# Optimization experiments

Measured on AMD Instinct MI355X. Metric: run time of the kernel, lower is better.

The kernel has to match this reference:

```python
import jax, jax.numpy as jnp
import numpy as np

TEMPERATURE = 0.07
NEG_INF = -1e30


def setup_inputs() -> dict:
    key = jax.random.key(0)
    k_h, k_m, k_l, k_w = jax.random.split(key, 4)
    B, L, H, P = 32, 1024, 1280, 128
    hidden_states = jax.random.normal(k_h, (B, L, H), dtype=jnp.float32)
    attention_mask = jax.random.randint(k_m, (B, L), 0, 2).astype(jnp.int32)
    labels = jax.random.randint(k_l, (B, L), 0, 4).astype(jnp.int32)
    proj_w = jax.random.normal(k_w, (H, P), dtype=jnp.float32) * 0.02
    proj_b = jnp.zeros((P,), dtype=jnp.float32)
    return {
        "hidden_states": hidden_states,
        "proj_w": proj_w,
        "proj_b": proj_b,
        "attention_mask": attention_mask,
        "labels": labels,
    }


def reference(hidden_states, proj_w, proj_b, attention_mask, labels):
    # Projection head (dropout is inactive at eval) + L2 normalize
    emb = hidden_states @ proj_w + proj_b                     # [B, L, P]
    emb = emb / jnp.linalg.norm(emb, axis=-1, keepdims=True)

    B, L, _ = emb.shape
    attn_valid = attention_mask.astype(bool)                  # [B, L]
    valid = attn_valid & (labels != -100)                     # anchor/candidate validity

    # Per-sequence token-token similarity, temperature-scaled
    sim = jnp.einsum("bip,bjp->bij", emb, emb) / TEMPERATURE  # [B, L, L]

    eye = jnp.eye(L, dtype=bool)                              # [L, L]
    col_valid = valid[:, None, :]                             # valid candidate j
    # Row max over valid columns (includes self, as in original filtered emb)
    m = jax.lax.stop_gradient(
        jnp.max(jnp.where(col_valid, sim, NEG_INF), axis=2, keepdims=True)
    )
    logits = sim - m
    logits_mask = col_valid & ~eye[None]                      # exclude self, invalid cols
    exp_logits = jnp.where(logits_mask, jnp.exp(logits), 0.0)
    log_prob = logits - jnp.log(exp_logits.sum(axis=2, keepdims=True) + 1e-12)

    # Positives: same label, same sequence, not self, both valid
    same_label = labels[:, :, None] == labels[:, None, :]
    pos_mask = (same_label & logits_mask & valid[:, :, None]).astype(sim.dtype)

    sum_pos_log_prob = (pos_mask * log_prob).sum(axis=2)      # [B, L]
    anchor_loss = sum_pos_log_prob / (pos_mask.sum(axis=2) + 1e-12)

    valid_f = valid.astype(sim.dtype)
    n_anchor = jnp.maximum(valid_f.sum(axis=1), 1.0)
    loss_seq = -(valid_f * anchor_loss).sum(axis=1) / n_anchor  # mean over valid anchors

    # Sequence included iff attention_mask has >= 2 valid tokens (original check)
    seq_ok = (attention_mask.sum(axis=1) >= 2)
    n_seq = jnp.maximum(seq_ok.sum().astype(sim.dtype), 1.0)
    loss = jnp.where(seq_ok, loss_seq, 0.0).sum() / n_seq
    return loss
```

## Files before the change

### kernel.cpp

```cpp
#include <hip/hip_runtime.h>
#include <hip/hip_bf16.h>
#include <cstddef>
#include <cstdint>

#define NB   32
#define LSEQ 1024
#define HDIM 1280
#define PDIM 128

typedef unsigned short ushort_t;
typedef __bf16 bf16x8 __attribute__((ext_vector_type(8)));
typedef float  f32x4  __attribute__((ext_vector_type(4)));

#define WT_OFF  256
#define E_OFF   (256 + HDIM * PDIM * 2)

__device__ __forceinline__ ushort_t bf16_rne(float x) {
  unsigned u = __float_as_uint(x);
  unsigned r = u + 0x7fffu + ((u >> 16) & 1u);
  return (ushort_t)(r >> 16);
}

__global__ __launch_bounds__(256) void k0_wt(const float* __restrict__ pw,
                                             ushort_t* __restrict__ wT,
                                             float* __restrict__ wsf) {
  if (blockIdx.x == 0 && threadIdx.x < 64) wsf[threadIdx.x] = 0.0f;
  const int idx = blockIdx.x * 256 + threadIdx.x;
  const int k = idx >> 7, n = idx & 127;
  wT[(size_t)n * HDIM + k] = bf16_rne(pw[(size_t)k * PDIM + n]);
}

__global__ __launch_bounds__(256, 4) void k1_mfma(const float* __restrict__ hs,
                                                  const ushort_t* __restrict__ wT,
                                                  const float* __restrict__ pb,
                                                  ushort_t* __restrict__ e) {
  __shared__ __align__(16) char smem[16 * HDIM * 2];
  ushort_t* Asm  = (ushort_t*)smem;
  float*    prtf = (float*)smem;

  const int tid = threadIdx.x;
  const int l = tid & 63, w = tid >> 6;
  const int lm = l & 15, lq = l >> 4;
  const int m0 = blockIdx.x * 16;
  const int k0 = w * 320;

  const ushort_t* brow = wT + (size_t)lm * HDIM + k0 + lq * 8;
  bf16x8 Bc[8], Bn[8];
#pragma unroll
  for (int t = 0; t < 8; ++t)
    Bc[t] = *(const bf16x8*)(brow + (size_t)t * 16 * HDIM);

  const float* prow = hs + (size_t)m0 * HDIM;
#pragma unroll
  for (int half = 0; half < 2; ++half) {
    const int r0 = w * 4 + half * 2;
    float4 buf[10];
#pragma unroll
    for (int rr = 0; rr < 2; ++rr)
#pragma unroll
      for (int i = 0; i < 5; ++i)
        buf[rr * 5 + i] =
            *(const float4*)(prow + (size_t)(r0 + rr) * HDIM + i * 256 + l * 4);
#pragma unroll
    for (int rr = 0; rr < 2; ++rr)
#pragma unroll
      for (int i = 0; i < 5; ++i) {
        const float4 v = buf[rr * 5 + i];
        union { ushort_t u[4]; uint2 p; } pk;
        pk.u[0] = bf16_rne(v.x); pk.u[1] = bf16_rne(v.y);
        pk.u[2] = bf16_rne(v.z); pk.u[3] = bf16_rne(v.w);
        *(uint2*)&Asm[(size_t)(r0 + rr) * HDIM + i * 256 + l * 4] = pk.p;
      }
  }
  __syncthreads();

  f32x4 acc[8];
#pragma unroll
  for (int t = 0; t < 8; ++t) acc[t] = (f32x4){0.f, 0.f, 0.f, 0.f};

#pragma unroll
  for (int s = 0; s < 10; ++s) {
    if (s < 9) {
#pragma unroll
      for (int t = 0; t < 8; ++t)
        Bn[t] = *(const bf16x8*)(brow + (size_t)t * 16 * HDIM + (s + 1) * 32);
    }
    const bf16x8 A = *(const bf16x8*)&Asm[(size_t)lm * HDIM + k0 + s * 32 + lq * 8];
#pragma unroll
    for (int t = 0; t < 8; ++t)
      acc[t] = __builtin_amdgcn_mfma_f32_16x16x32_bf16(A, Bc[t], acc[t], 0, 0, 0);
#pragma unroll
    for (int t = 0; t < 8; ++t) Bc[t] = Bn[t];
  }

  __syncthreads();
#define PART(pp, row, col) prtf[((pp) * 16 + (row)) * 132 + (col)]
  if (w < 2) {
#pragma unroll
    for (int t = 0; t < 8; ++t)
#pragma unroll
      for (int r = 0; r < 4; ++r)
        PART(w, lq * 4 + r, t * 16 + lm) = acc[t][r];
  }
  __syncthreads();
  if (w >= 2) {
#pragma unroll
    for (int t = 0; t < 8; ++t)
#pragma unroll
      for (int r = 0; r < 4; ++r)
        PART(w - 2, lq * 4 + r, t * 16 + lm) += acc[t][r];
  }
  __syncthreads();

  const int row = w * 4 + lq;
  float val[8];
  float s2 = 0.f;
#pragma unroll
  for (int t = 0; t < 8; ++t) {
    val[t] = PART(0, row, t * 16 + lm) + PART(1, row, t * 16 + lm) +
             pb[t * 16 + lm];
    s2 = fmaf(val[t], val[t], s2);
  }
  s2 += __shfl_xor(s2, 1, 64);
  s2 += __shfl_xor(s2, 2, 64);
  s2 += __shfl_xor(s2, 4, 64);
  s2 += __shfl_xor(s2, 8, 64);
  const float inv = 1.0f / sqrtf(s2);
#pragma unroll
  for (int t = 0; t < 8; ++t)
    e[(size_t)(m0 + row) * PDIM + t * 16 + lm] = bf16_rne(val[t] * inv);
#undef PART
}

__global__ __launch_bounds__(256, 3) void k2_loss(const ushort_t* __restrict__ e,
                                                  const int* __restrict__ mask,
                                                  const int* __restrict__ labels,
                                                  float* __restrict__ accb) {
  __shared__ float part[4][32][3];

  const int tid = threadIdx.x;
  const int l = tid & 63, w = tid >> 6;
  const int b  = blockIdx.x >> 5;
  const int i0 = (blockIdx.x & 31) << 5;
  const int lm = l & 15, lq = l >> 4;

  const ushort_t* eb   = e + (size_t)b * LSEQ * PDIM;
  const int*      mrow = mask + b * LSEQ;
  const int*      lrow = labels + b * LSEQ;

  bf16x8 af[2][4];
#pragma unroll
  for (int ii = 0; ii < 2; ++ii) {
    const ushort_t* aptr = eb + (size_t)(i0 + ii * 16 + lm) * PDIM + lq * 8;
#pragma unroll
    for (int c = 0; c < 4; ++c) af[ii][c] = *(const bf16x8*)(aptr + c * 32);
  }

  int  li[2][4], ar[2][4];
  bool vi[2][4];
#pragma unroll
  for (int ii = 0; ii < 2; ++ii)
#pragma unroll
    for (int r = 0; r < 4; ++r) {
      ar[ii][r] = i0 + ii * 16 + lq * 4 + r;
      li[ii][r] = lrow[ar[ii][r]];
      vi[ii][r] = (mrow[ar[ii][r]] != 0) && (li[ii][r] != -100);
    }

  float d[2][4] = {}, ps[2][4] = {}, pc[2][4] = {};
  const float invT = 1.0f / 0.07f;

  int jt = w * 16;
  bf16x8 Bc[4];
  int ljc, mjc;
  {
    const int j = jt * 16 + lm;
    const ushort_t* bptr = eb + (size_t)j * PDIM + lq * 8;
#pragma unroll
    for (int c = 0; c < 4; ++c) Bc[c] = *(const bf16x8*)(bptr + c * 32);
    ljc = lrow[j];
    mjc = mrow[j];
  }

#pragma unroll 1
  for (int s = 0; s < 16; ++s, ++jt) {
    bf16x8 Bn[4];
    int ljn = 0, mjn = 0;
    if (s < 15) {
      const int jn = (jt + 1) * 16 + lm;
      const ushort_t* bptr = eb + (size_t)jn * PDIM + lq * 8;
#pragma unroll
      for (int c = 0; c < 4; ++c) Bn[c] = *(const bf16x8*)(bptr + c * 32);
      ljn = lrow[jn];
      mjn = mrow[jn];
    }

    const int j = jt * 16 + lm;
    const bool cvj = (mjc != 0) && (ljc != -100);
#pragma unroll
    for (int ii = 0; ii < 2; ++ii) {
      f32x4 acc = (f32x4){0.f, 0.f, 0.f, 0.f};
#pragma unroll
      for (int c = 0; c < 4; ++c)
        acc = __builtin_amdgcn_mfma_f32_16x16x32_bf16(af[ii][c], Bc[c], acc, 0, 0, 0);
#pragma unroll
      for (int r = 0; r < 4; ++r) {
        const float sv = acc[r] * invT;
        const bool dm  = cvj && (j != ar[ii][r]);
        const float ex = __expf(sv);
        d[ii][r] += dm ? ex : 0.f;
        const bool pos = dm && (ljc == li[ii][r]) && vi[ii][r];
        ps[ii][r] += pos ? sv : 0.f;
        pc[ii][r] += pos ? 1.f : 0.f;
      }
    }

#pragma unroll
    for (int c = 0; c < 4; ++c) Bc[c] = Bn[c];
    ljc = ljn; mjc = mjn;
  }

#pragma unroll
  for (int ii = 0; ii < 2; ++ii)
#pragma unroll
    for (int r = 0; r < 4; ++r) {
#pragma unroll
      for (int off = 1; off < 16; off <<= 1) {
        d[ii][r]  += __shfl_xor(d[ii][r], off, 64);
        ps[ii][r] += __shfl_xor(ps[ii][r], off, 64);
        pc[ii][r] += __shfl_xor(pc[ii][r], off, 64);
      }
    }
  if (lm == 0) {
#pragma unroll
    for (int ii = 0; ii < 2; ++ii)
#pragma unroll
      for (int r = 0; r < 4; ++r) {
        part[w][ii * 16 + lq * 4 + r][0] = d[ii][r];
        part[w][ii * 16 + lq * 4 + r][1] = ps[ii][r];
        part[w][ii * 16 + lq * 4 + r][2] = pc[ii][r];
      }
  }
  __syncthreads();

  if (tid < 32) {
    float D = 0.f, P = 0.f, C = 0.f;
#pragma unroll
    for (int w2 = 0; w2 < 4; ++w2) {
      D += part[w2][tid][0];
      P += part[w2][tid][1];
      C += part[w2][tid][2];
    }
    const float logD = logf(D + 1e-12f);
    float al = (P - C * logD) / (C + 1e-12f);
#pragma unroll
    for (int off = 1; off < 32; off <<= 1) al += __shfl_xor(al, off, 64);
    if (tid == 0) atomicAdd(&accb[b], al);
  }
}

__global__ __launch_bounds__(1024) void k3_final(const int* __restrict__ mask,
                                                 const int* __restrict__ labels,
                                                 const float* __restrict__ accb,
                                                 float* __restrict__ out) {
  __shared__ float lossv[NB];
  __shared__ float okv[NB];
  const int t = threadIdx.x;
  const int b = t >> 5, sub = t & 31;

  int cm = 0, cv = 0;
#pragma unroll
  for (int q = 0; q < 8; ++q) {
    const int idx = b * LSEQ + q * 128 + sub * 4;
    const int4 mv = *(const int4*)(mask + idx);
    const int4 lv = *(const int4*)(labels + idx);
    cm += mv.x + mv.y + mv.z + mv.w;
    cv += ((mv.x != 0 && lv.x != -100) ? 1 : 0) +
          ((mv.y != 0 && lv.y != -100) ? 1 : 0) +
          ((mv.z != 0 && lv.z != -100) ? 1 : 0) +
          ((mv.w != 0 && lv.w != -100) ? 1 : 0);
  }
#pragma unroll
  for (int off = 16; off; off >>= 1) {
    cm += __shfl_xor(cm, off, 64);
    cv += __shfl_xor(cv, off, 64);
  }
  if (sub == 0) {
    const bool ok = (cm >= 2);
    lossv[b] = ok ? (-accb[b] / fmaxf((float)cv, 1.0f)) : 0.0f;
    okv[b]   = ok ? 1.0f : 0.0f;
  }
  __syncthreads();
  if (t < NB) {
    float lv = lossv[t], ov = okv[t];
#pragma unroll
    for (int off = 16; off; off >>= 1) {
      lv += __shfl_xor(lv, off, 64);
      ov += __shfl_xor(ov, off, 64);
    }
    if (t == 0) out[0] = lv / fmaxf(ov, 1.0f);
  }
}

extern "C" void kernel_launch(void* const* d_in, const int* in_sizes, int n_in,
                              void* d_out, int out_size, void* d_ws, size_t ws_size,
                              hipStream_t stream) {
  (void)in_sizes; (void)n_in; (void)out_size; (void)ws_size;
  const float* hs     = (const float*)d_in[0];
  const float* pw     = (const float*)d_in[1];
  const float* pb     = (const float*)d_in[2];
  const int*   mask   = (const int*)d_in[3];
  const int*   labels = (const int*)d_in[4];
  float* out = (float*)d_out;

  char* wsb = (char*)d_ws;
  float*    wsf  = (float*)wsb;
  float*    accb = wsf;
  ushort_t* wT   = (ushort_t*)(wsb + WT_OFF);
  ushort_t* e    = (ushort_t*)(wsb + E_OFF);

  k0_wt<<<(HDIM * PDIM) / 256, 256, 0, stream>>>(pw, wT, wsf);
  k1_mfma<<<(NB * LSEQ) / 16, 256, 0, stream>>>(hs, wT, pb, e);
  k2_loss<<<NB * 32, 256, 0, stream>>>(e, mask, labels, accb);
  k3_final<<<1, 1024, 0, stream>>>(mask, labels, accb, out);
}
```

Measured before the change: 343.3 us.

## Restructure projection GEMM as single-wave blocks with pre-swizzled weights and register pipelining

The weight matrix is now written by k0 in an MFMA-fragment-ordered layout, so each lane loads contiguous bf16x8 B fragments. k1 runs one 64-thread wave per 16-row tile and walks the full K dimension itself. The fp32 hidden states are loaded straight into registers with a 4-deep prefetch and converted to bf16 on the fly, which removes the LDS staging, the cross-wave K-split reduction and the barriers. In exchange each wave now runs a 40-step serial chain with fewer waves per block, so latency hiding depends on occupancy and the register prefetch.

```diff
diff --git a/kernel.cpp b/kernel.cpp
--- a/kernel.cpp
+++ b/kernel.cpp
@@ -7,6 +7,7 @@
 #define LSEQ 1024
 #define HDIM 1280
 #define PDIM 128
+#define KCHUNKS 40
 
 typedef unsigned short ushort_t;
 typedef __bf16 bf16x8 __attribute__((ext_vector_type(8)));
@@ -22,114 +23,96 @@
 }
 
 __global__ __launch_bounds__(256) void k0_wt(const float* __restrict__ pw,
-                                             ushort_t* __restrict__ wT,
+                                             ushort_t* __restrict__ wB,
                                              float* __restrict__ wsf) {
   if (blockIdx.x == 0 && threadIdx.x < 64) wsf[threadIdx.x] = 0.0f;
   const int idx = blockIdx.x * 256 + threadIdx.x;
   const int k = idx >> 7, n = idx & 127;
-  wT[(size_t)n * HDIM + k] = bf16_rne(pw[(size_t)k * PDIM + n]);
-}
-
-__global__ __launch_bounds__(256, 4) void k1_mfma(const float* __restrict__ hs,
-                                                  const ushort_t* __restrict__ wT,
-                                                  const float* __restrict__ pb,
-                                                  ushort_t* __restrict__ e) {
-  __shared__ __align__(16) char smem[16 * HDIM * 2];
-  ushort_t* Asm  = (ushort_t*)smem;
-  float*    prtf = (float*)smem;
-
-  const int tid = threadIdx.x;
-  const int l = tid & 63, w = tid >> 6;
+  const int kc = k >> 5, kr = k & 31;
+  const int t = n >> 4, lm = n & 15;
+  const int lq = kr >> 3, j = kr & 7;
+  const int l = lq * 16 + lm;
+  wB[((size_t)(kc * 8 + t) * 64 + l) * 8 + j] = bf16_rne(pw[(size_t)k * PDIM + n]);
+}
+
+__global__ __launch_bounds__(64, 2) void k1_mfma(const float* __restrict__ hs,
+                                                 const ushort_t* __restrict__ wB,
+                                                 const float* __restrict__ pb,
+                                                 ushort_t* __restrict__ e) {
+  const int l = threadIdx.x;
   const int lm = l & 15, lq = l >> 4;
   const int m0 = blockIdx.x * 16;
-  const int k0 = w * 320;
-
-  const ushort_t* brow = wT + (size_t)lm * HDIM + k0 + lq * 8;
-  bf16x8 Bc[8], Bn[8];
-#pragma unroll
-  for (int t = 0; t < 8; ++t)
-    Bc[t] = *(const bf16x8*)(brow + (size_t)t * 16 * HDIM);
-
-  const float* prow = hs + (size_t)m0 * HDIM;
-#pragma unroll
-  for (int half = 0; half < 2; ++half) {
-    const int r0 = w * 4 + half * 2;
-    float4 buf[10];
-#pragma unroll
-    for (int rr = 0; rr < 2; ++rr)
-#pragma unroll
-      for (int i = 0; i < 5; ++i)
-        buf[rr * 5 + i] =
-            *(const float4*)(prow + (size_t)(r0 + rr) * HDIM + i * 256 + l * 4);
-#pragma unroll
-    for (int rr = 0; rr < 2; ++rr)
-#pragma unroll
-      for (int i = 0; i < 5; ++i) {
-        const float4 v = buf[rr * 5 + i];
-        union { ushort_t u[4]; uint2 p; } pk;
-        pk.u[0] = bf16_rne(v.x); pk.u[1] = bf16_rne(v.y);
-        pk.u[2] = bf16_rne(v.z); pk.u[3] = bf16_rne(v.w);
-        *(uint2*)&Asm[(size_t)(r0 + rr) * HDIM + i * 256 + l * 4] = pk.p;
-      }
-  }
-  __syncthreads();
+
+  const float*    arow  = hs + (size_t)(m0 + lm) * HDIM + lq * 8;
+  const ushort_t* bbase = wB + (size_t)l * 8;
+
+  float4 Abuf[4][2];
+#pragma unroll
+  for (int d = 0; d < 4; ++d) {
+    Abuf[d][0] = *(const float4*)(arow + d * 32);
+    Abuf[d][1] = *(const float4*)(arow + d * 32 + 4);
+  }
+  bf16x8 Bc[8], Bn[8], Bm[8];
+#pragma unroll
+  for (int t = 0; t < 8; ++t) {
+    Bc[t] = *(const bf16x8*)(bbase + (size_t)(0 * 8 + t) * 512);
+    Bn[t] = *(const bf16x8*)(bbase + (size_t)(1 * 8 + t) * 512);
+  }
 
   f32x4 acc[8];
 #pragma unroll
   for (int t = 0; t < 8; ++t) acc[t] = (f32x4){0.f, 0.f, 0.f, 0.f};
 
-#pragma unroll
-  for (int s = 0; s < 10; ++s) {
-    if (s < 9) {
-#pragma unroll
-      for (int t = 0; t < 8; ++t)
-        Bn[t] = *(const bf16x8*)(brow + (size_t)t * 16 * HDIM + (s + 1) * 32);
-    }
-    const bf16x8 A = *(const bf16x8*)&Asm[(size_t)lm * HDIM + k0 + s * 32 + lq * 8];
+#pragma unroll 4
+  for (int kc = 0; kc < KCHUNKS; ++kc) {
+    const int kb = (kc + 2 < KCHUNKS) ? kc + 2 : KCHUNKS - 1;
 #pragma unroll
     for (int t = 0; t < 8; ++t)
-      acc[t] = __builtin_amdgcn_mfma_f32_16x16x32_bf16(A, Bc[t], acc[t], 0, 0, 0);
-#pragma unroll
-    for (int t = 0; t < 8; ++t) Bc[t] = Bn[t];
-  }
-
-  __syncthreads();
-#define PART(pp, row, col) prtf[((pp) * 16 + (row)) * 132 + (col)]
-  if (w < 2) {
+      Bm[t] = *(const bf16x8*)(bbase + (size_t)(kb * 8 + t) * 512);
+
+    union { ushort_t u[8]; bf16x8 v; } cv;
+    const float4 f0 = Abuf[kc & 3][0];
+    const float4 f1 = Abuf[kc & 3][1];
+    cv.u[0] = bf16_rne(f0.x); cv.u[1] = bf16_rne(f0.y);
+    cv.u[2] = bf16_rne(f0.z); cv.u[3] = bf16_rne(f0.w);
+    cv.u[4] = bf16_rne(f1.x); cv.u[5] = bf16_rne(f1.y);
+    cv.u[6] = bf16_rne(f1.z); cv.u[7] = bf16_rne(f1.w);
+    const bf16x8 a = cv.v;
+
+    const int ka = (kc + 4 < KCHUNKS) ? kc + 4 : KCHUNKS - 1;
+    Abuf[kc & 3][0] = *(const float4*)(arow + ka * 32);
+    Abuf[kc & 3][1] = *(const float4*)(arow + ka * 32 + 4);
+
 #pragma unroll
     for (int t = 0; t < 8; ++t)
-#pragma unroll
-      for (int r = 0; r < 4; ++r)
-        PART(w, lq * 4 + r, t * 16 + lm) = acc[t][r];
-  }
-  __syncthreads();
-  if (w >= 2) {
-#pragma unroll
-    for (int t = 0; t < 8; ++t)
-#pragma unroll
-      for (int r = 0; r < 4; ++r)
-        PART(w - 2, lq * 4 + r, t * 16 + lm) += acc[t][r];
-  }
-  __syncthreads();
-
-  const int row = w * 4 + lq;
-  float val[8];
-  float s2 = 0.f;
-#pragma unroll
-  for (int t = 0; t < 8; ++t) {
-    val[t] = PART(0, row, t * 16 + lm) + PART(1, row, t * 16 + lm) +
-             pb[t * 16 + lm];
-    s2 = fmaf(val[t], val[t], s2);
-  }
-  s2 += __shfl_xor(s2, 1, 64);
-  s2 += __shfl_xor(s2, 2, 64);
-  s2 += __shfl_xor(s2, 4, 64);
-  s2 += __shfl_xor(s2, 8, 64);
-  const float inv = 1.0f / sqrtf(s2);
-#pragma unroll
-  for (int t = 0; t < 8; ++t)
-    e[(size_t)(m0 + row) * PDIM + t * 16 + lm] = bf16_rne(val[t] * inv);
-#undef PART
+      acc[t] = __builtin_amdgcn_mfma_f32_16x16x32_bf16(a, Bc[t], acc[t], 0, 0, 0);
+
+#pragma unroll
+    for (int t = 0; t < 8; ++t) { Bc[t] = Bn[t]; Bn[t] = Bm[t]; }
+  }
+
+  float pbv[8];
+#pragma unroll
+  for (int t = 0; t < 8; ++t) pbv[t] = pb[t * 16 + lm];
+
+#pragma unroll
+  for (int r = 0; r < 4; ++r) {
+    float v[8];
+    float s2 = 0.f;
+#pragma unroll
+    for (int t = 0; t < 8; ++t) {
+      v[t] = acc[t][r] + pbv[t];
+      s2 = fmaf(v[t], v[t], s2);
+    }
+    s2 += __shfl_xor(s2, 1, 64);
+    s2 += __shfl_xor(s2, 2, 64);
+    s2 += __shfl_xor(s2, 4, 64);
+    s2 += __shfl_xor(s2, 8, 64);
+    const float inv = 1.0f / sqrtf(s2);
+    ushort_t* erow = e + (size_t)(m0 + lq * 4 + r) * PDIM + lm;
+#pragma unroll
+    for (int t = 0; t < 8; ++t) erow[t * 16] = bf16_rne(v[t] * inv);
+  }
 }
 
 __global__ __launch_bounds__(256, 3) void k2_loss(const ushort_t* __restrict__ e,
@@ -316,11 +299,11 @@
   char* wsb = (char*)d_ws;
   float*    wsf  = (float*)wsb;
   float*    accb = wsf;
-  ushort_t* wT   = (ushort_t*)(wsb + WT_OFF);
+  ushort_t* wB   = (ushort_t*)(wsb + WT_OFF);
   ushort_t* e    = (ushort_t*)(wsb + E_OFF);
 
-  k0_wt<<<(HDIM * PDIM) / 256, 256, 0, stream>>>(pw, wT, wsf);
-  k1_mfma<<<(NB * LSEQ) / 16, 256, 0, stream>>>(hs, wT, pb, e);
+  k0_wt<<<(HDIM * PDIM) / 256, 256, 0, stream>>>(pw, wB, wsf);
+  k1_mfma<<<(NB * LSEQ) / 16, 64, 0, stream>>>(hs, wB, pb, e);
   k2_loss<<<NB * 32, 256, 0, stream>>>(e, mask, labels, accb);
   k3_final<<<1, 1024, 0, stream>>>(mask, labels, accb, out);
 }
```

Result: faster. 314.8 us (-8.3%).
